# Optimization experiments

Hardware: AMD Instinct MI355X
Metric: run time of the kernel (lower is better)

The kernel has to match this reference:

```python
import jax, jax.numpy as jnp
import numpy as np

GAMMA_MAX = 0.5  # config.gamma_max


def setup_inputs() -> dict:
    key = jax.random.key(0)
    ks = jax.random.split(key, 12)
    B, T, NC, Nc, Dn, A, Hm = 8, 16, 128, 64, 64, 4, 128
    inp = {}
    inp["x"] = jax.random.normal(ks[0], (B, T, NC, Dn), jnp.float32)
    inp["h0"] = jnp.zeros((B, NC, Nc, Dn), jnp.float32)
    inp["W0"] = jax.random.normal(ks[1], (B, NC, Nc, Nc), jnp.float32) * (Nc ** -0.5)
    inp["hebbian0"] = jnp.zeros((B, NC, Nc, Nc), jnp.float32)
    inp["neuron_id"] = jax.random.normal(ks[2], (NC, Nc, Dn), jnp.float32) * (Dn ** -0.5)
    inp["msg_w1"] = jax.random.normal(ks[3], (Hm, Dn), jnp.float32) * (Dn ** -0.5)
    inp["msg_b1"] = jnp.zeros((Hm,), jnp.float32)
    inp["msg_w2"] = jax.random.normal(ks[4], (Dn, Hm), jnp.float32) * (Hm ** -0.5)
    inp["msg_b2"] = jnp.zeros((Dn,), jnp.float32)
    inp["inject_w"] = jax.random.normal(ks[5], (NC, A * Dn, Dn), jnp.float32) * (Dn ** -0.5)
    inp["inject_b"] = jnp.zeros((NC, A * Dn), jnp.float32)
    inp["W_decay_logit"] = jnp.full((NC, Nc), -3.0, jnp.float32) + 0.1 * jax.random.normal(ks[6], (NC, Nc))
    inp["decay_gamma_logit"] = jnp.full((NC, Nc), -3.0, jnp.float32) + 0.1 * jax.random.normal(ks[7], (NC, Nc))
    inp["hebbian_decay_logit"] = jnp.full((NC, Nc), 2.0, jnp.float32) + 0.1 * jax.random.normal(ks[8], (NC, Nc))
    inp["input_port_idx"] = jax.random.randint(ks[9], (NC, A), 0, Nc, jnp.int32)
    inp["output_port_idx"] = jax.random.randint(ks[10], (NC, A), 0, Nc, jnp.int32)
    return inp


def _forward(x, h0, W0, hebbian0, neuron_id, msg_w1, msg_b1, msg_w2, msg_b2,
             inject_w, inject_b, W_decay_logit, decay_gamma_logit,
             hebbian_decay_logit, input_port_idx, output_port_idx):
    B, T, NC, Dn = x.shape
    Nc = h0.shape[2]
    A = inject_b.shape[1] // Dn
    cell = jnp.arange(NC)[:, None]            # [NC,1], broadcasts with [NC,A] ports
    eye = jnp.eye(Nc, dtype=h0.dtype)
    gamma = GAMMA_MAX * jax.nn.sigmoid(decay_gamma_logit)[..., None]    # [NC,Nc,1] state gate
    hg = GAMMA_MAX * jax.nn.sigmoid(hebbian_decay_logit)[..., None]     # hebbian plasticity rate
    wg = GAMMA_MAX * jax.nn.sigmoid(W_decay_logit)[..., None]           # slow-weight decay
    ro_scale = A ** -0.5                       # readout_scale = alpha**-0.5

    def step(carry, xt):
        h, W, heb = carry
        # per-cell injection: D_n -> alpha*D_n, scattered onto input ports
        inj = (jnp.einsum('bcd,ckd->bck', xt, inject_w) + inject_b).reshape(B, NC, A, Dn)
        h_in = h.at[:, cell, input_port_idx].add(inj)
        # recurrent message passing through fast weights (W + hebbian): per-cell NcxNc matmul
        m = jnp.einsum('bcij,bcjd->bcid', W + heb, h_in)
        # shared message MLP (tanh hidden)
        m = jnp.tanh(m @ msg_w1.T + msg_b1) @ msg_w2.T + msg_b2
        # per-neuron gated state update
        h_new = (1.0 - gamma) * h_in + gamma * jnp.tanh(m + neuron_id)
        # Hebbian outer-product fast-weight update, off-diagonal only
        a = h_new * (Dn ** -0.5)
        heb_new = ((1.0 - hg) * heb + hg * jnp.einsum('bcid,bcjd->bcij', a, a)) * (1.0 - eye)
        W_new = (1.0 - wg) * W
        # readout from output ports
        ro = h_new[:, cell, output_port_idx].mean(axis=2) * ro_scale   # [B,NC,Dn]
        return (h_new, W_new, heb_new), ro.reshape(B, NC * Dn)

    _, ros = jax.lax.scan(step, (h0, W0, hebbian0), jnp.swapaxes(x, 0, 1))
    return jnp.swapaxes(ros, 0, 1)             # [B, T, NC*Dn]


def reference(x, h0, W0, hebbian0, neuron_id, msg_w1, msg_b1, msg_w2, msg_b2,
              inject_w, inject_b, W_decay_logit, decay_gamma_logit,
              hebbian_decay_logit, input_port_idx, output_port_idx):
    return _forward(x, h0, W0, hebbian0, neuron_id, msg_w1, msg_b1, msg_w2, msg_b2,
                    inject_w, inject_b, W_decay_logit, decay_gamma_logit,
                    hebbian_decay_logit, input_port_idx, output_port_idx)
```

## Files before the change

kernel.cpp:

```cpp
#include <hip/hip_runtime.h>
#include <math.h>

namespace {

typedef __attribute__((ext_vector_type(8))) short bf16x8;
typedef __attribute__((ext_vector_type(4))) float f32x4;

constexpr int NCg = 128;

__device__ inline short bfr(float f) {
    unsigned u = __float_as_uint(f);
    unsigned r = (u + 0x7fffu + ((u >> 16) & 1u)) >> 16;
    return (short)r;
}
__device__ inline float bf2f(short s) {
    return __uint_as_float(((unsigned)(unsigned short)s) << 16);
}
__device__ inline unsigned pack2(float a, float b) {
    return (unsigned)(unsigned short)bfr(a) | ((unsigned)(unsigned short)bfr(b) << 16);
}
__device__ inline float tanh_f(float x) {
    float t = __builtin_amdgcn_exp2f(x * 2.8853900817779268f);
    return 1.0f - 2.0f * __builtin_amdgcn_rcpf(t + 1.0f);
}
__device__ inline float sig05(float x) { return 0.5f / (1.0f + expf(-x)); }

__device__ inline bf16x8 ld64(const short* base, int row, int kbyte) {
    int byte = (row << 7) + kbyte; byte ^= (row & 7) << 4;
    return *(const bf16x8*)((const char*)base + byte);
}
__device__ inline bf16x8 ld128(const short* base, int row, int kbyte) {
    int byte = (row << 8) + kbyte; byte ^= (row & 7) << 4;
    return *(const bf16x8*)((const char*)base + byte);
}
__device__ inline short* p16_64(short* base, int row, int col) {
    int byte = (row << 7) + (col << 1); byte ^= (row & 7) << 4;
    return (short*)((char*)base + byte);
}
__device__ inline unsigned long long ldnb(const short* base, int row, int colbyte) {
    int byte = (row << 7) + colbyte; byte ^= (row & 7) << 4;
    return *(const unsigned long long*)((const char*)base + byte);
}
__device__ inline void st32_64(short* base, int row, int col, unsigned v) {
    int byte = (row << 7) + (col << 1); byte ^= (row & 7) << 4;
    *(unsigned*)((char*)base + byte) = v;
}
__device__ inline void st32_128(short* base, int row, int col, unsigned v) {
    int byte = (row << 8) + (col << 1); byte ^= (row & 7) << 4;
    *(unsigned*)((char*)base + byte) = v;
}
#define MFMA(a,b,c) __builtin_amdgcn_mfma_f32_16x16x32_bf16(a, b, c, 0, 0, 0)
#define PIN(v) asm volatile("" : "+v"(v))

__global__ void cvt_w12(const float* __restrict__ w2, const float* __restrict__ w1,
                        short* __restrict__ w2b, short* __restrict__ w1b) {
    int e = blockIdx.x * 256 + threadIdx.x;
    if (e < 8192) w2b[e] = bfr(w2[e]);
    else          w1b[e - 8192] = bfr(w1[e - 8192]);
}

__global__ __launch_bounds__(256) void inj_gemm(
    const float* __restrict__ x,
    const float* __restrict__ injw,
    const float* __restrict__ injb,
    float* __restrict__ inj)
{
    const int c = blockIdx.x;
    const int p = threadIdx.x;
    float w[64];
    const float* wr = injw + ((size_t)c * 256 + p) * 64;
    #pragma unroll
    for (int k = 0; k < 64; k += 4) {
        float4 v = *(const float4*)(wr + k);
        w[k] = v.x; w[k+1] = v.y; w[k+2] = v.z; w[k+3] = v.w;
    }
    const float bias = injb[c * 256 + p];
    __shared__ float xs[16][64];
    #pragma unroll 1
    for (int chunk = 0; chunk < 8; ++chunk) {
        const int bt0 = chunk * 16;
        {
            int e = threadIdx.x * 4;
            *(float4*)&xs[e >> 6][e & 63] =
                *(const float4*)(x + ((size_t)(bt0 + (e >> 6)) * NCg + c) * 64 + (e & 63));
        }
        __syncthreads();
        #pragma unroll 1
        for (int r = 0; r < 16; ++r) {
            float acc = bias;
            #pragma unroll
            for (int k = 0; k < 64; ++k) acc = fmaf(w[k], xs[r][k], acc);
            inj[((size_t)(bt0 + r) * NCg + c) * 256 + p] = acc;
        }
        __syncthreads();
    }
}

__global__ __launch_bounds__(256, 3) void memgraph_mfma(
    const float* __restrict__ inj,    const float* __restrict__ h0,
    const float* __restrict__ W0,     const float* __restrict__ heb0,
    const float* __restrict__ nid,    const short* __restrict__ w1b,
    const float* __restrict__ b1,     const short* __restrict__ w2b,
    const float* __restrict__ b2,     const float* __restrict__ wdl,
    const float* __restrict__ dgl,    const float* __restrict__ hdl,
    const int*  __restrict__ iport,   const int*  __restrict__ oport,
    float* __restrict__ out)
{
    __shared__ short heb_s[4096];
    __shared__ short hinT_s[4096];
    __shared__ short mh_s[4096];
    __shared__ short nbT_s[4096];
    __shared__ short hidA_s[8192] __attribute__((aligned(16)));

    const int bc  = blockIdx.x;
    const int b   = bc >> 7;
    const int c   = bc & (NCg - 1);
    const int tid = threadIdx.x;
    const int Wv  = tid >> 6;
    const int l   = tid & 63;
    const int g   = l >> 4;
    const int lm  = l & 15;
    const int rowC = 16 * Wv + 4 * g;
    const int rowA = 16 * Wv + lm;
    const int kb0  = 16 * g;

    const size_t cellBase = (size_t)bc;

    const float* hb0p = heb0 + cellBase * 4096;
    #pragma unroll
    for (int u = 0; u < 16; ++u) {
        int e = tid + 256 * u;
        *p16_64(heb_s, e >> 6, e & 63) = bfr(hb0p[e]);
    }

    float gi4[4], hg4[4], w0a[16];
    #pragma unroll
    for (int r = 0; r < 4; ++r) {
        gi4[r] = sig05(dgl[c * 64 + rowC + r]);
        hg4[r] = sig05(hdl[c * 64 + rowC + r]);
    }
    float wdecA = 1.0f - sig05(wdl[c * 64 + rowA]);
    float wpowA = 1.0f;
    {
        const float* w0row = W0 + cellBase * 4096 + (size_t)rowA * 64;
        #pragma unroll
        for (int jj = 0; jj < 8; ++jj) {
            w0a[jj]     = w0row[8 * g + jj];
            w0a[8 + jj] = w0row[32 + 8 * g + jj];
        }
    }
    #pragma unroll
    for (int k = 0; k < 16; ++k) PIN(w0a[k]);
    #pragma unroll
    for (int k = 0; k < 4; ++k)  { PIN(gi4[k]); PIN(hg4[k]); }
    PIN(wdecA);

    #pragma unroll
    for (int nt = 0; nt < 4; ++nt)
        #pragma unroll
        for (int r = 0; r < 4; ++r) {
            int d = lm + 16 * nt, i = rowC + r;
            *p16_64(nbT_s, d, i) = bfr(b2[d] + nid[((size_t)c * 64 + i) * 64 + d]);
        }

    int ip4[4], op4[4];
    #pragma unroll
    for (int a = 0; a < 4; ++a) { ip4[a] = iport[c * 4 + a]; op4[a] = oport[c * 4 + a]; }

    float hreg[16];
    {
        const float* h0c = h0 + cellBase * 4096;
        const float* ir0 = inj + (((size_t)b * 16) * NCg + c) * 256 + l;
        float injv0[4];
        #pragma unroll
        for (int a = 0; a < 4; ++a) injv0[a] = ir0[a * 64];
        #pragma unroll
        for (int nt = 0; nt < 4; ++nt) {
            int d = lm + 16 * nt;
            float iv[4];
            #pragma unroll
            for (int a = 0; a < 4; ++a) iv[a] = __shfl(injv0[a], d);
            #pragma unroll
            for (int r = 0; r < 4; ++r) {
                int i = rowC + r;
                float add = 0.0f;
                #pragma unroll
                for (int a = 0; a < 4; ++a) add += (ip4[a] == i) ? iv[a] : 0.0f;
                hreg[nt * 4 + r] = h0c[(size_t)i * 64 + d] + add;
            }
        }
    }
    #pragma unroll
    for (int nt = 0; nt < 4; ++nt)
        #pragma unroll
        for (int r = 0; r < 4; ++r)
            *p16_64(hidA_s, rowC + r, lm + 16 * nt) = bfr(hreg[nt * 4 + r]);
    __syncthreads();
    {
        int d = tid >> 2, q = tid & 3;
        #pragma unroll
        for (int k = 0; k < 16; k += 2) {
            int col = 16 * q + k;
            st32_64(hinT_s, d, col,
                    pack2(bf2f(*p16_64(hidA_s, col, d)),
                          bf2f(*p16_64(hidA_s, col + 1, d))));
        }
    }
    __syncthreads();

    const f32x4 zf = {0.f, 0.f, 0.f, 0.f};

    #pragma unroll 1
    for (int t = 0; t < 16; ++t) {
        int go = 0; asm volatile("" : "+v"(go));

        f32x4 acc2[4] = {zf, zf, zf, zf};
        {
            bf16x8 hb0 = ld64(heb_s, rowA, kb0);
            bf16x8 hb1 = ld64(heb_s, rowA, kb0 + 64);
            bf16x8 a0, a1;
            #pragma unroll
            for (int jj = 0; jj < 8; ++jj) {
                a0[jj] = bfr(fmaf(wpowA, w0a[jj],     bf2f(hb0[jj])));
                a1[jj] = bfr(fmaf(wpowA, w0a[8 + jj], bf2f(hb1[jj])));
            }
            #pragma unroll
            for (int nt = 0; nt < 4; ++nt) {
                bf16x8 bb0 = ld64(hinT_s, lm + 16 * nt, kb0);
                bf16x8 bb1 = ld64(hinT_s, lm + 16 * nt, kb0 + 64);
                acc2[nt] = MFMA(a0, bb0, acc2[nt]);
                acc2[nt] = MFMA(a1, bb1, acc2[nt]);
            }
        }
        #pragma unroll
        for (int nt = 0; nt < 4; ++nt)
            #pragma unroll
            for (int r = 0; r < 4; ++r)
                *p16_64(mh_s, rowC + r, lm + 16 * nt) = bfr(acc2[nt][r]);
        __syncthreads();

        float injv[4];
        {
            int tn = (t < 15) ? t + 1 : 15;
            const float* ir = inj + (((size_t)(b * 16 + tn)) * NCg + c) * 256 + l;
            #pragma unroll
            for (int a = 0; a < 4; ++a) injv[a] = ir[a * 64];
        }

        #pragma unroll
        for (int mt = 0; mt < 2; ++mt) {
            bf16x8 awf0 = *(const bf16x8*)(w1b + ((32 * Wv + 16 * mt + lm) << 6) + 8 * g + go);
            bf16x8 awf1 = *(const bf16x8*)(w1b + ((32 * Wv + 16 * mt + lm) << 6) + 8 * g + 32 + go);
            float4 b1f = *(const float4*)(b1 + 32 * Wv + 16 * mt + 4 * g + go);
            float b1a[4] = {b1f.x, b1f.y, b1f.z, b1f.w};
            #pragma unroll
            for (int nt = 0; nt < 4; ++nt) {
                f32x4 a3 = zf;
                a3 = MFMA(awf0, ld64(mh_s, lm + 16 * nt, kb0),      a3);
                a3 = MFMA(awf1, ld64(mh_s, lm + 16 * nt, kb0 + 64), a3);
                float v0 = tanh_f(a3[0] + b1a[0]);
                float v1 = tanh_f(a3[1] + b1a[1]);
                float v2 = tanh_f(a3[2] + b1a[2]);
                float v3 = tanh_f(a3[3] + b1a[3]);
                st32_128(hidA_s, lm + 16 * nt, 32 * Wv + 16 * mt + 4 * g + 0, pack2(v0, v1));
                st32_128(hidA_s, lm + 16 * nt, 32 * Wv + 16 * mt + 4 * g + 2, pack2(v2, v3));
            }
        }
        __syncthreads();

        f32x4 accB[4] = {zf, zf, zf, zf};
        {
            bf16x8 ah[4];
            #pragma unroll
            for (int kt = 0; kt < 4; ++kt)
                ah[kt] = ld128(hidA_s, 16 * Wv + lm, kb0 + 64 * kt);
            #pragma unroll
            for (int kt = 0; kt < 4; ++kt)
                #pragma unroll
                for (int nt = 0; nt < 4; ++nt) {
                    const short* w2r = w2b + ((lm + 16 * nt) << 7) + 8 * g + 32 * kt + go;
                    bf16x8 bb = *(const bf16x8*)w2r;
                    accB[nt] = MFMA(ah[kt], bb, accB[nt]);
                }
        }

        #pragma unroll
        for (int nt = 0; nt < 4; ++nt) {
            int d = lm + 16 * nt;
            unsigned long long nbq = ldnb(nbT_s, d, rowC << 1);
            float iv[4];
            #pragma unroll
            for (int a = 0; a < 4; ++a) iv[a] = __shfl(injv[a], d);
            float hv[4];
            #pragma unroll
            for (int r = 0; r < 4; ++r) {
                int i = rowC + r;
                float nb = bf2f((short)(nbq >> (16 * r)));
                float tv = tanh_f(accB[nt][r] + nb);
                hv[r] = (1.0f - gi4[r]) * hreg[nt * 4 + r] + gi4[r] * tv;
                *p16_64(mh_s, i, d) = bfr(hv[r]);
                float add = 0.0f;
                #pragma unroll
                for (int a = 0; a < 4; ++a) add += (ip4[a] == i) ? iv[a] : 0.0f;
                hreg[nt * 4 + r] = hv[r] + add;
            }
            st32_64(hinT_s, d, rowC,     pack2(hreg[nt * 4 + 0], hreg[nt * 4 + 1]));
            st32_64(hinT_s, d, rowC + 2, pack2(hreg[nt * 4 + 2], hreg[nt * 4 + 3]));
        }
        __syncthreads();

        f32x4 acc6[4] = {zf, zf, zf, zf};
        {
            bf16x8 ha0 = ld64(mh_s, rowA, kb0);
            bf16x8 ha1 = ld64(mh_s, rowA, kb0 + 64);
            #pragma unroll
            for (int nt = 0; nt < 4; ++nt) {
                bf16x8 bb0 = ld64(mh_s, lm + 16 * nt, kb0);
                bf16x8 bb1 = ld64(mh_s, lm + 16 * nt, kb0 + 64);
                acc6[nt] = MFMA(ha0, bb0, acc6[nt]);
                acc6[nt] = MFMA(ha1, bb1, acc6[nt]);
            }
        }
        if (tid < 64) {
            float ro = 0.125f * (bf2f(*p16_64(mh_s, op4[0], tid)) +
                                 bf2f(*p16_64(mh_s, op4[1], tid)) +
                                 bf2f(*p16_64(mh_s, op4[2], tid)) +
                                 bf2f(*p16_64(mh_s, op4[3], tid)));
            out[(((size_t)b * 16 + t) * NCg + c) * 64 + tid] = ro;
        }
        #pragma unroll
        for (int nt = 0; nt < 4; ++nt)
            #pragma unroll
            for (int r = 0; r < 4; ++r) {
                int i = rowC + r, j = lm + 16 * nt;
                short* hb = p16_64(heb_s, i, j);
                float nv = (1.0f - hg4[r]) * bf2f(*hb) + hg4[r] * (acc6[nt][r] * 0.015625f);
                *hb = (j == i) ? (short)0 : bfr(nv);
            }
        wpowA *= wdecA;
        __syncthreads();
    }
}

}

extern "C" void kernel_launch(void* const* d_in, const int* in_sizes, int n_in,
                              void* d_out, int out_size, void* d_ws, size_t ws_size,
                              hipStream_t stream) {
    (void)in_sizes; (void)n_in; (void)out_size; (void)ws_size;
    const float* x    = (const float*)d_in[0];
    const float* h0   = (const float*)d_in[1];
    const float* W0   = (const float*)d_in[2];
    const float* heb0 = (const float*)d_in[3];
    const float* nid  = (const float*)d_in[4];
    const float* w1   = (const float*)d_in[5];
    const float* b1   = (const float*)d_in[6];
    const float* w2   = (const float*)d_in[7];
    const float* b2   = (const float*)d_in[8];
    const float* injw = (const float*)d_in[9];
    const float* injb = (const float*)d_in[10];
    const float* wdl  = (const float*)d_in[11];
    const float* dgl  = (const float*)d_in[12];
    const float* hdl  = (const float*)d_in[13];
    const int*   ip   = (const int*)d_in[14];
    const int*   op   = (const int*)d_in[15];
    float* out = (float*)d_out;

    char* ws = (char*)d_ws;
    short* w2b = (short*)(ws + 0);
    short* w1b = (short*)(ws + 16384);
    float* inj = (float*)(ws + 65536);

    cvt_w12<<<dim3(64), dim3(256), 0, stream>>>(w2, w1, w2b, w1b);
    inj_gemm<<<dim3(128), dim3(256), 0, stream>>>(x, injw, injb, inj);
    memgraph_mfma<<<dim3(8 * NCg), dim3(256), 0, stream>>>(
        inj, h0, W0, heb0, nid, w1b, b1, w2b, b2,
        wdl, dgl, hdl, ip, op, out);
}
```

Before: 384.0 us.

## Precompute neuron bias table in global memory to free LDS and raise occupancy

A new pre-pass kernel writes the bf16 sum of b2 and neuron_id into a per-thread layout in workspace. The main kernel reads it with two 16-byte global loads per step instead of building and reading an LDS table. This removes 8 KB of shared memory per block and raises the occupancy hint from 3 to 4 blocks per CU. In exchange there is per-step global/L2 traffic, a tighter register budget that may cause spills, and one extra kernel launch.

New measurement: 516.5 us. 34.5% more time.

```diff
diff --git a/kernel.cpp b/kernel.cpp
--- a/kernel.cpp
+++ b/kernel.cpp
@@ -36,10 +36,6 @@
 __device__ inline short* p16_64(short* base, int row, int col) {
     int byte = (row << 7) + (col << 1); byte ^= (row & 7) << 4;
     return (short*)((char*)base + byte);
-}
-__device__ inline unsigned long long ldnb(const short* base, int row, int colbyte) {
-    int byte = (row << 7) + colbyte; byte ^= (row & 7) << 4;
-    return *(const unsigned long long*)((const char*)base + byte);
 }
 __device__ inline void st32_64(short* base, int row, int col, unsigned v) {
     int byte = (row << 7) + (col << 1); byte ^= (row & 7) << 4;
@@ -57,6 +53,25 @@
     int e = blockIdx.x * 256 + threadIdx.x;
     if (e < 8192) w2b[e] = bfr(w2[e]);
     else          w1b[e - 8192] = bfr(w1[e - 8192]);
+}
+
+__global__ __launch_bounds__(256) void build_nbt(
+    const float* __restrict__ nid,
+    const float* __restrict__ b2,
+    short* __restrict__ nbt)
+{
+    const int c   = blockIdx.x;
+    const int tid = threadIdx.x;
+    const int Wv = tid >> 6, l = tid & 63, g = l >> 4, lm = l & 15;
+    const int rowC = 16 * Wv + 4 * g;
+    short* dst = nbt + ((size_t)c * 256 + tid) * 16;
+    #pragma unroll
+    for (int nt = 0; nt < 4; ++nt) {
+        int d = lm + 16 * nt;
+        #pragma unroll
+        for (int r = 0; r < 4; ++r)
+            dst[nt * 4 + r] = bfr(b2[d] + nid[((size_t)c * 64 + rowC + r) * 64 + d]);
+    }
 }
 
 __global__ __launch_bounds__(256) void inj_gemm(
@@ -96,12 +111,12 @@
     }
 }
 
-__global__ __launch_bounds__(256, 3) void memgraph_mfma(
+__global__ __launch_bounds__(256, 4) void memgraph_mfma(
     const float* __restrict__ inj,    const float* __restrict__ h0,
     const float* __restrict__ W0,     const float* __restrict__ heb0,
-    const float* __restrict__ nid,    const short* __restrict__ w1b,
+    const short* __restrict__ nbt,    const short* __restrict__ w1b,
     const float* __restrict__ b1,     const short* __restrict__ w2b,
-    const float* __restrict__ b2,     const float* __restrict__ wdl,
+    const float* __restrict__ wdl,
     const float* __restrict__ dgl,    const float* __restrict__ hdl,
     const int*  __restrict__ iport,   const int*  __restrict__ oport,
     float* __restrict__ out)
@@ -109,7 +124,6 @@
     __shared__ short heb_s[4096];
     __shared__ short hinT_s[4096];
     __shared__ short mh_s[4096];
-    __shared__ short nbT_s[4096];
     __shared__ short hidA_s[8192] __attribute__((aligned(16)));
 
     const int bc  = blockIdx.x;
@@ -155,17 +169,11 @@
     for (int k = 0; k < 4; ++k)  { PIN(gi4[k]); PIN(hg4[k]); }
     PIN(wdecA);
 
-    #pragma unroll
-    for (int nt = 0; nt < 4; ++nt)
-        #pragma unroll
-        for (int r = 0; r < 4; ++r) {
-            int d = lm + 16 * nt, i = rowC + r;
-            *p16_64(nbT_s, d, i) = bfr(b2[d] + nid[((size_t)c * 64 + i) * 64 + d]);
-        }
-
     int ip4[4], op4[4];
     #pragma unroll
     for (int a = 0; a < 4; ++a) { ip4[a] = iport[c * 4 + a]; op4[a] = oport[c * 4 + a]; }
+
+    const short* nbp = nbt + ((size_t)c * 256 + tid) * 16;
 
     float hreg[16];
     {
@@ -284,28 +292,31 @@
                 }
         }
 
-        #pragma unroll
-        for (int nt = 0; nt < 4; ++nt) {
-            int d = lm + 16 * nt;
-            unsigned long long nbq = ldnb(nbT_s, d, rowC << 1);
-            float iv[4];
-            #pragma unroll
-            for (int a = 0; a < 4; ++a) iv[a] = __shfl(injv[a], d);
-            float hv[4];
-            #pragma unroll
-            for (int r = 0; r < 4; ++r) {
-                int i = rowC + r;
-                float nb = bf2f((short)(nbq >> (16 * r)));
-                float tv = tanh_f(accB[nt][r] + nb);
-                hv[r] = (1.0f - gi4[r]) * hreg[nt * 4 + r] + gi4[r] * tv;
-                *p16_64(mh_s, i, d) = bfr(hv[r]);
-                float add = 0.0f;
+        {
+            bf16x8 nbv0 = *(const bf16x8*)(nbp + go);
+            bf16x8 nbv1 = *(const bf16x8*)(nbp + 8 + go);
+            #pragma unroll
+            for (int nt = 0; nt < 4; ++nt) {
+                int d = lm + 16 * nt;
+                float iv[4];
                 #pragma unroll
-                for (int a = 0; a < 4; ++a) add += (ip4[a] == i) ? iv[a] : 0.0f;
-                hreg[nt * 4 + r] = hv[r] + add;
-            }
-            st32_64(hinT_s, d, rowC,     pack2(hreg[nt * 4 + 0], hreg[nt * 4 + 1]));
-            st32_64(hinT_s, d, rowC + 2, pack2(hreg[nt * 4 + 2], hreg[nt * 4 + 3]));
+                for (int a = 0; a < 4; ++a) iv[a] = __shfl(injv[a], d);
+                float hv[4];
+                #pragma unroll
+                for (int r = 0; r < 4; ++r) {
+                    int i = rowC + r;
+                    float nb = bf2f(nt < 2 ? nbv0[nt * 4 + r] : nbv1[(nt - 2) * 4 + r]);
+                    float tv = tanh_f(accB[nt][r] + nb);
+                    hv[r] = (1.0f - gi4[r]) * hreg[nt * 4 + r] + gi4[r] * tv;
+                    *p16_64(mh_s, i, d) = bfr(hv[r]);
+                    float add = 0.0f;
+                    #pragma unroll
+                    for (int a = 0; a < 4; ++a) add += (ip4[a] == i) ? iv[a] : 0.0f;
+                    hreg[nt * 4 + r] = hv[r] + add;
+                }
+                st32_64(hinT_s, d, rowC,     pack2(hreg[nt * 4 + 0], hreg[nt * 4 + 1]));
+                st32_64(hinT_s, d, rowC + 2, pack2(hreg[nt * 4 + 2], hreg[nt * 4 + 3]));
+            }
         }
         __syncthreads();
 
@@ -369,11 +380,13 @@
     char* ws = (char*)d_ws;
     short* w2b = (short*)(ws + 0);
     short* w1b = (short*)(ws + 16384);
-    float* inj = (float*)(ws + 65536);
+    short* nbt = (short*)(ws + 32768);
+    float* inj = (float*)(ws + 1081344);
 
     cvt_w12<<<dim3(64), dim3(256), 0, stream>>>(w2, w1, w2b, w1b);
+    build_nbt<<<dim3(128), dim3(256), 0, stream>>>(nid, b2, nbt);
     inj_gemm<<<dim3(128), dim3(256), 0, stream>>>(x, injw, injb, inj);
     memgraph_mfma<<<dim3(8 * NCg), dim3(256), 0, stream>>>(
-        inj, h0, W0, heb0, nid, w1b, b1, w2b, b2,
+        inj, h0, W0, heb0, nbt, w1b, b1, w2b,
         wdl, dgl, hdl, ip, op, out);
 }
```
